# Kernel tuning notes

Measured on AMD Instinct MI355X. Metric: run time of the kernel, lower is better.

## Reference

```python
import jax, jax.numpy as jnp
import numpy as np

DIM = 2048
HQ = 32
HKV = 8
HEAD_DIM = DIM // HQ          # 64
GROUP = HQ // HKV             # 4 q-heads per kv-head
B, S = 2, 2048


def setup_inputs() -> dict:
    key = jax.random.key(0)
    ks = jax.random.split(key, 12)
    sc_in = 1.0 / np.sqrt(DIM)   # lecun_normal fan-in scaling
    inp = {
        "q": jax.random.normal(ks[0], (B, S, DIM), jnp.float32),
        "k": jax.random.normal(ks[1], (B, S, DIM), jnp.float32),
        "v": jax.random.normal(ks[2], (B, S, DIM), jnp.float32),
        # causal 0/1 mask: module computes scores -= 1/mask + 1, so 0 -> -inf (masked), 1 -> -2 (softmax-invariant shift)
        "mask": jnp.tril(jnp.ones((S, S), jnp.int32)),
        "Wq": jax.random.normal(ks[3], (DIM, HQ * HEAD_DIM), jnp.float32) * sc_in,
        "bq": jnp.zeros((HQ * HEAD_DIM,), jnp.float32),
        "Wk": jax.random.normal(ks[4], (DIM, HKV * HEAD_DIM), jnp.float32) * sc_in,
        "bk": jnp.zeros((HKV * HEAD_DIM,), jnp.float32),
        "Wv": jax.random.normal(ks[5], (DIM, HKV * HEAD_DIM), jnp.float32) * sc_in,
        "bv": jnp.zeros((HKV * HEAD_DIM,), jnp.float32),
        "Wo": jax.random.normal(ks[6], (DIM, DIM), jnp.float32) * (1.0 / np.sqrt(DIM)),
        "bo": jnp.zeros((DIM,), jnp.float32),
    }
    return inp


def reference(q, k, v, mask, Wq, bq, Wk, bk, Wv, bv, Wo, bo):
    b, s, _ = q.shape
    # projections -> per-head layout
    qx = (q @ Wq + bq).reshape(b, s, HKV, GROUP, HEAD_DIM)   # grouped q-heads
    kx = (k @ Wk + bk).reshape(b, s, HKV, HEAD_DIM)
    vx = (v @ Wv + bv).reshape(b, s, HKV, HEAD_DIM)
    # scores[b, h, g, i, j] = q_i . k_j ; same math as repeating kv heads GROUP times
    scores = jnp.einsum('bihgd,bjhd->bhgij', qx, kx) / jnp.sqrt(
        jnp.asarray(HEAD_DIM, qx.dtype))
    # module's masking: scores -= 1/mask + 1  (mask==0 -> -inf, mask==1 -> -2)
    scores = scores - (1.0 / mask.astype(scores.dtype) + 1.0)
    probs = jax.nn.softmax(scores, axis=-1)
    out = jnp.einsum('bhgij,bjhd->bihgd', probs, vx).reshape(b, s, DIM)
    out = out @ Wo + bo
    return out
```

## Files before the change

kernel.cpp:

```cpp
#include <hip/hip_runtime.h>

typedef unsigned short u16;
typedef unsigned int u32;
typedef __attribute__((ext_vector_type(8))) short short8v;
typedef __attribute__((ext_vector_type(4))) float f32x4;

#define DIM 2048
#define HQN 32
#define HKVN 8
#define HD 64
#define BB 2
#define SS 2048
#define MTOT (BB*SS)
#define NKV (HKVN*HD)
#define QSCL 0.18033688011112042f

__device__ __forceinline__ u16 f2bf(float f){
  u32 u = __float_as_uint(f);
  u += 0x7FFFu + ((u >> 16) & 1u);
  return (u16)(u >> 16);
}

__device__ __forceinline__ u32 cvtpk(float a, float b){
  u32 r; asm("v_cvt_pk_bf16_f32 %0, %1, %2" : "=v"(r) : "v"(a), "v"(b)); return r;
}

__device__ __forceinline__ void gload_lds16(const void* g, void* l){
  __builtin_amdgcn_global_load_lds((const __attribute__((address_space(1))) u32*)g,
                                   (__attribute__((address_space(3))) u32*)l, 16, 0, 0);
}

#define WAITVM_(N) asm volatile("s_waitcnt vmcnt(" #N ")" ::: "memory")
#define WAITVM(N) WAITVM_(N)
#define BARF()    do { asm volatile("" ::: "memory"); __builtin_amdgcn_s_barrier(); asm volatile("" ::: "memory"); } while(0)
#define MF(a,b,cc) __builtin_amdgcn_mfma_f32_16x16x32_bf16((a),(b),(cc),0,0,0)

__global__ __launch_bounds__(256) void cast3_kernel(const float4* __restrict__ q,
                                                    const float4* __restrict__ k,
                                                    const float4* __restrict__ v,
                                                    u16* __restrict__ qo,
                                                    u16* __restrict__ ko,
                                                    u16* __restrict__ vo, int n4){
  const int z = blockIdx.y;
  const float4* in = z==0 ? q : (z==1 ? k : v);
  u16* out = z==0 ? qo : (z==1 ? ko : vo);
  int i = blockIdx.x*256 + threadIdx.x;
  if (i < n4){
    float4 f = in[i];
    union { u16 s[4]; unsigned long long u; } r;
    r.s[0]=f2bf(f.x); r.s[1]=f2bf(f.y); r.s[2]=f2bf(f.z); r.s[3]=f2bf(f.w);
    *(unsigned long long*)(out + (size_t)i*4) = r.u;
  }
}

__global__ __launch_bounds__(256) void transpose4_kernel(const float* __restrict__ Wq,
                                                         const float* __restrict__ Wk,
                                                         const float* __restrict__ Wv,
                                                         const float* __restrict__ Wo,
                                                         u16* __restrict__ WqT,
                                                         u16* __restrict__ WkT,
                                                         u16* __restrict__ WvT,
                                                         u16* __restrict__ WoT){
  const int z = blockIdx.z;
  const float* W = z==0?Wq:(z==1?Wk:(z==2?Wv:Wo));
  u16* WT = z==0?WqT:(z==1?WkT:(z==2?WvT:WoT));
  const int N = (z==1||z==2) ? NKV : DIM;
  const int K = DIM;
  int n0 = blockIdx.x*32, k0 = blockIdx.y*32;
  if (n0 >= N) return;
  __shared__ float tile[32][33];
  int tx = threadIdx.x & 31, ty = threadIdx.x >> 5;
  #pragma unroll
  for (int i=0;i<4;i++){
    int kk = ty + i*8;
    tile[kk][tx] = W[(size_t)(k0+kk)*N + n0 + tx];
  }
  __syncthreads();
  #pragma unroll
  for (int i=0;i<4;i++){
    int n = ty + i*8;
    WT[(size_t)(n0+n)*K + k0 + tx] = f2bf(tile[tx][n]);
  }
}

__global__ __launch_bounds__(512, 1) void gemm_qkv_kernel(const u16* __restrict__ Aq,
                                                          const u16* __restrict__ Ak,
                                                          const u16* __restrict__ Av,
                                                          const u16* __restrict__ BT,
                                                          const float* __restrict__ bq,
                                                          const float* __restrict__ bk,
                                                          const float* __restrict__ bv,
                                                          u16* __restrict__ Qp,
                                                          u16* __restrict__ Kp,
                                                          u16* __restrict__ Vp){
  __shared__ __align__(16) u16 lds[65536];
  char* ldsb = (char*)lds;
  const int t = threadIdx.x, lane = t & 63, w = t >> 6;
  const int wm = w >> 2, wn = w & 3, g = lane >> 4, c = lane & 15;
  int bid = blockIdx.x;
  bid = (bid & 7)*24 + (bid >> 3);
  const int mt = bid / 12, nt = bid - mt*12;
  const int m0 = mt*256, n0 = nt*256;
  const int seg = (n0 >= 2560) ? 2 : (n0 >= 2048 ? 1 : 0);
  const u16* A = seg==0 ? Aq : (seg==1 ? Ak : Av);
  const float* bias = seg==0 ? bq : (seg==1 ? bk : bv);
  const int nbase = seg==0 ? 0 : (seg==1 ? 2048 : 2560);

  const int rA = t >> 3;
  const int kc = ((t & 7) ^ (rA & 7)) * 8;
  const u16* gA = A  + (size_t)(m0 + rA)*DIM + kc;
  const u16* gB = BT + (size_t)(n0 + ((rA>>5)<<6) + (rA & 31))*DIM + kc;

  const u32 ko0 = (u32)((g*16) ^ ((c&7)<<4));
  const u32 ko1 = (u32)((64 + g*16) ^ ((c&7)<<4));
  const u32 aoff = wm*8192 + c*128;
  const u32 boff = wn*4096 + c*128;

#define STGA_(PA, KT, ABASE) do{ \
    gload_lds16(gA + (size_t)(KT)*64 + (size_t)((PA)*64)*DIM,       ldsb + (ABASE) + (PA)*16384 + t*16); \
    gload_lds16(gA + (size_t)(KT)*64 + (size_t)((PA)*64+128)*DIM,   ldsb + (ABASE) + (PA)*16384 + 8192 + t*16); }while(0)
#define STGB_(PB, KT, BBASE) do{ \
    gload_lds16(gB + (size_t)(KT)*64 + (size_t)((PB)*32)*DIM,       ldsb + (BBASE) + (PB)*16384 + t*16); \
    gload_lds16(gB + (size_t)(KT)*64 + (size_t)((PB)*32+128)*DIM,   ldsb + (BBASE) + (PB)*16384 + 8192 + t*16); }while(0)
#define LD8(OFF) (*(const short8v*)(ldsb + (OFF)))

  const f32x4 fzero = {0.f,0.f,0.f,0.f};
  f32x4 acc[8][4];
  #pragma unroll
  for (int i=0;i<8;i++)
    #pragma unroll
    for (int j=0;j<4;j++) acc[i][j] = fzero;

#define RD_A(PABASE) do{ _Pragma("unroll") for (int q=0;q<4;q++){ \
    a_[q][0] = LD8((PABASE) + aoff + q*2048 + ko0); \
    a_[q][1] = LD8((PABASE) + aoff + q*2048 + ko1); } }while(0)
#define RD_B(DST, PBBASE) do{ _Pragma("unroll") for (int s=0;s<2;s++){ \
    DST[s][0] = LD8((PBBASE) + boff + s*2048 + ko0); \
    DST[s][1] = LD8((PBBASE) + boff + s*2048 + ko1); } }while(0)

#define MM16(BSRC, FM0, FN0) do{ __builtin_amdgcn_s_setprio(1); \
    _Pragma("unroll") for (int q=0;q<4;q++) \
      _Pragma("unroll") for (int s=0;s<2;s++){ \
        acc[(FM0)+q][(FN0)+s] = MF(a_[q][0], BSRC[s][0], acc[(FM0)+q][(FN0)+s]); \
        acc[(FM0)+q][(FN0)+s] = MF(a_[q][1], BSRC[s][1], acc[(FM0)+q][(FN0)+s]); } \
    __builtin_amdgcn_s_setprio(0); }while(0)

#define QSTEP(TT, CUR, DOSTG, TAIL) do{ \
    const u32 AC = (CUR)*32768,  BC2 = 65536 + (CUR)*32768; \
    const u32 AN = (CUR^1)*32768, BN2 = 65536 + (CUR^1)*32768; \
    short8v a_[4][2], b0_[2][2], b1_[2][2]; \
     \
    RD_A(AC); RD_B(b0_, BC2); \
    if (DOSTG) STGA_(0, (TT)+1, AN); \
    MM16(b0_, 0, 0); \
    if (TAIL) { WAITVM(2); } else { WAITVM(4); } \
    BARF(); \
     \
    RD_B(b1_, BC2 + 16384); \
    if (DOSTG) STGB_(0, (TT)+1, BN2); \
    MM16(b1_, 0, 2); \
    if (TAIL) { WAITVM(0); } else { WAITVM(4); } \
    BARF(); \
     \
    RD_A(AC + 16384); \
    if (DOSTG) STGB_(1, (TT)+1, BN2); \
    MM16(b1_, 4, 2); \
    BARF(); \
     \
    if (DOSTG) STGA_(1, (TT)+1, AN); \
    MM16(b0_, 4, 0); \
    if (!TAIL) { WAITVM(4); } \
    BARF(); \
  }while(0)

  STGA_(0, 0, 0); STGB_(0, 0, 65536); STGB_(1, 0, 65536); STGA_(1, 0, 0);
  WAITVM(4);
  BARF();

  #pragma unroll 1
  for (int tt = 0; tt < 30; tt += 2){
    QSTEP(tt,   0, 1, 0);
    QSTEP(tt+1, 1, 1, 0);
  }
  QSTEP(30, 0, 1, 0);
  QSTEP(31, 1, 0, 1);
#undef QSTEP

  WAITVM(0);
  __syncthreads();

  u16* st = lds + w*8192;
  const float osc = (seg == 0) ? QSCL : 1.0f;
  if (seg == 2){
    #pragma unroll
    for (int fm=0; fm<8; fm++){
      #pragma unroll
      for (int fn=0; fn<4; fn++){
        float bvv = bias[n0 - nbase + wn*64 + fn*16 + c];
        int vbase = (fm>>1)*2048 + fn*512 + (g*16 + c)*8 + (fm&1)*4;
        *(u32*)&st[vbase]     = cvtpk(acc[fm][fn][0]+bvv, acc[fm][fn][1]+bvv);
        *(u32*)&st[vbase + 2] = cvtpk(acc[fm][fn][2]+bvv, acc[fm][fn][3]+bvv);
      }
    }
  } else {
    #pragma unroll
    for (int fm=0; fm<8; fm++){
      #pragma unroll
      for (int fn=0; fn<4; fn++){
        float bvv = bias[n0 - nbase + wn*64 + fn*16 + c];
        int sbase = (fm>>1)*2048 + ((fm&1)*2 + (fn>>1))*512 + (c>>2)*128 + (fn&1)*4 + (c&3);
        #pragma unroll
        for (int r=0; r<4; r++)
          st[sbase + (4*g + r)*8] = f2bf((acc[fm][fn][r] + bvv)*osc);
      }
    }
  }
  __syncthreads();
  {
    const int bb = m0 >> 11;
    const int st0 = ((m0 & 2047) >> 5) + wm*4;
    u16* dst;
    if (seg == 0)      dst = Qp + (((size_t)bb*HQN  + (n0>>6)        + wn) << 17);
    else if (seg == 1) dst = Kp + (((size_t)bb*HKVN + ((n0-2048)>>6) + wn) << 17);
    else               dst = Vp + (((size_t)bb*HKVN + ((n0-2560)>>6) + wn) << 17);
    dst += (size_t)st0*2048;
    #pragma unroll
    for (int i=0;i<16;i++)
      *(short8v*)(dst + lane*8 + i*512) = *(const short8v*)(st + lane*8 + i*512);
  }
#undef STGA_
#undef STGB_
#undef RD_A
#undef RD_B
#undef MM16
}

__global__ __launch_bounds__(512, 1) void gemm_o_kernel(const u16* __restrict__ A,
                                                        const u16* __restrict__ BT,
                                                        const float* __restrict__ bias,
                                                        float* __restrict__ C){
  __shared__ __align__(16) u16 lds[49152];
  char* ldsb = (char*)lds;
  const int t = threadIdx.x, lane = t & 63, w = t >> 6;
  const int wm = w >> 2, wn = w & 3, g = lane >> 4, c = lane & 15;
  int bid = blockIdx.x;
  bid = (bid & 7)*32 + (bid >> 3);
  const int m0 = (bid >> 4)*256, n0 = (bid & 15)*128;

  const int rA = t >> 3;
  const int kc = ((t & 7) ^ (rA & 7)) * 8;
  const u16* gA = A  + (size_t)(m0 + rA)*DIM + kc;
  const u16* gB = BT + (size_t)(n0 + rA)*DIM + kc;

  const u32 ko0 = (u32)((g*16) ^ ((c&7)<<4));
  const u32 ko1 = (u32)((64 + g*16) ^ ((c&7)<<4));
  const u32 aoff = wm*8192 + c*128;
  const u32 boffo = wn*4096 + c*128;

#define STGA_(PA, KT, ABASE) do{ \
    gload_lds16(gA + (size_t)(KT)*64 + (size_t)((PA)*64)*DIM,       ldsb + (ABASE) + (PA)*16384 + t*16); \
    gload_lds16(gA + (size_t)(KT)*64 + (size_t)((PA)*64+128)*DIM,   ldsb + (ABASE) + (PA)*16384 + 8192 + t*16); }while(0)
#define STGB_O(KT, BBASE) do{ \
    gload_lds16(gB + (size_t)(KT)*64,                     ldsb + (BBASE) + t*16); \
    gload_lds16(gB + (size_t)(KT)*64 + (size_t)64*DIM,    ldsb + (BBASE) + 8192 + t*16); }while(0)
#define LD8(OFF) (*(const short8v*)(ldsb + (OFF)))

  const f32x4 fzero = {0.f,0.f,0.f,0.f};
  f32x4 acc[8][2];
  #pragma unroll
  for (int i=0;i<8;i++){ acc[i][0] = fzero; acc[i][1] = fzero; }

#define RD_A(PABASE) do{ _Pragma("unroll") for (int q=0;q<4;q++){ \
    a_[q][0] = LD8((PABASE) + aoff + q*2048 + ko0); \
    a_[q][1] = LD8((PABASE) + aoff + q*2048 + ko1); } }while(0)
#define RD_BO(BBASE) do{ _Pragma("unroll") for (int s=0;s<2;s++){ \
    b_[s][0] = LD8((BBASE) + boffo + s*2048 + ko0); \
    b_[s][1] = LD8((BBASE) + boffo + s*2048 + ko1); } }while(0)

#define MMO(FM0) do{ __builtin_amdgcn_s_setprio(1); \
    _Pragma("unroll") for (int q=0;q<4;q++) \
      _Pragma("unroll") for (int s=0;s<2;s++){ \
        acc[(FM0)+q][s] = MF(a_[q][0], b_[s][0], acc[(FM0)+q][s]); \
        acc[(FM0)+q][s] = MF(a_[q][1], b_[s][1], acc[(FM0)+q][s]); } \
    __builtin_amdgcn_s_setprio(0); }while(0)

#define OSTEP(TT, CUR, DOSTG, TAIL) do{ \
    const u32 AC = (CUR)*32768,  BC2 = 65536 + (CUR)*16384; \
    const u32 AN = (CUR^1)*32768, BN2 = 65536 + (CUR^1)*16384; \
    short8v a_[4][2], b_[2][2]; \
     \
    RD_A(AC); RD_BO(BC2); \
    if (DOSTG) { STGA_(0, (TT)+1, AN); STGB_O((TT)+1, BN2); } \
    MMO(0); \
    if (TAIL) { WAITVM(0); } else { WAITVM(4); } \
    BARF(); \
     \
    RD_A(AC + 16384); \
    if (DOSTG) STGA_(1, (TT)+1, AN); \
    MMO(4); \
    if (!TAIL) { WAITVM(2); } \
    BARF(); \
  }while(0)

  STGA_(0, 0, 0); STGB_O(0, 65536); STGA_(1, 0, 0);
  WAITVM(2);
  BARF();

  #pragma unroll 1
  for (int tt = 0; tt < 30; tt += 2){
    OSTEP(tt,   0, 1, 0);
    OSTEP(tt+1, 1, 1, 0);
  }
  OSTEP(30, 0, 1, 0);
  OSTEP(31, 1, 0, 1);
#undef OSTEP

  #pragma unroll
  for (int fm=0; fm<8; fm++){
    #pragma unroll
    for (int s=0; s<2; s++){
      int n = n0 + wn*32 + s*16 + c;
      float bvv = bias[n];
      #pragma unroll
      for (int r=0; r<4; r++){
        int m = m0 + wm*128 + fm*16 + 4*g + r;
        C[(size_t)m*DIM + n] = acc[fm][s][r] + bvv;
      }
    }
  }
#undef STGA_
#undef STGB_O
#undef RD_A
#undef RD_BO
#undef MMO
}

__global__ __launch_bounds__(256) void attn_kernel(const u16* __restrict__ Qp,
                                                   const u16* __restrict__ Kp,
                                                   const u16* __restrict__ Vp,
                                                   u16* __restrict__ Aout){
  const int bid = blockIdx.x;
  const int grp = bid & 15;
  const int T   = 63 - (bid >> 4);
  const int b   = grp >> 3;
  const int hkv = grp & 7;
  const int t = threadIdx.x;
  const int lane = t & 63, w = t >> 6;
  const int g = lane >> 4, c = lane & 15;
  const int hq = hkv*4 + w;

  __shared__ __align__(16) u16 ring[4][2][2048];

  const u16* Kb = Kp + (((size_t)b*HKVN + hkv) << 17);
  const u16* Vb = Vp + (((size_t)b*HKVN + hkv) << 17);
  const u16* Qb = Qp + (((size_t)b*HQN + hq) << 17);
  const f32x4 fzero = {0.f,0.f,0.f,0.f};

  short8v qf[2][2];
  {
    const u16* qs = Qb + (size_t)T*2048 + lane*8;
    qf[0][0] = *(const short8v*)(qs);
    qf[0][1] = *(const short8v*)(qs + 512);
    qf[1][0] = *(const short8v*)(qs + 1024);
    qf[1][1] = *(const short8v*)(qs + 1536);
  }
  float l_r[2] = {0.f, 0.f};
  f32x4 o[2][4];
  #pragma unroll
  for (int qi=0; qi<2; qi++)
    #pragma unroll
    for (int f=0; f<4; f++) o[qi][f] = fzero;

  #pragma unroll
  for (int s=0; s<3; s++){
    const int tc = s > T ? T : s;
    gload_lds16(Kb + (size_t)tc*2048 + t*8, &ring[s][0][t*8]);
    gload_lds16(Vb + (size_t)tc*2048 + t*8, &ring[s][1][t*8]);
  }

  for (int kt = 0; kt <= T; kt += 4){
    #pragma unroll
    for (int s4 = 0; s4 < 4; ++s4){
      const int kt_ = kt + s4;
      if (kt_ > T) break;
      WAITVM(4);
      BARF();
      short8v kf0 = *(const short8v*)&ring[s4][0][lane*8];
      short8v kf1 = *(const short8v*)&ring[s4][0][512 + lane*8];
      short8v kf2 = *(const short8v*)&ring[s4][0][1024 + lane*8];
      short8v kf3 = *(const short8v*)&ring[s4][0][1536 + lane*8];
      short8v vf0 = *(const short8v*)&ring[s4][1][lane*8];
      short8v vf1 = *(const short8v*)&ring[s4][1][512 + lane*8];
      short8v vf2 = *(const short8v*)&ring[s4][1][1024 + lane*8];
      short8v vf3 = *(const short8v*)&ring[s4][1][1536 + lane*8];
      {
        const int tc = (kt_+3) > T ? T : (kt_+3);
        const int sn = (s4+3) & 3;
        gload_lds16(Kb + (size_t)tc*2048 + t*8, &ring[sn][0][t*8]);
        gload_lds16(Vb + (size_t)tc*2048 + t*8, &ring[sn][1][t*8]);
      }
      const bool diag = (kt_ == T);
      #pragma unroll
      for (int qi=0; qi<2; qi++){
        f32x4 s0 = fzero, s1 = fzero;
        __builtin_amdgcn_s_setprio(1);
        s0 = MF(kf0, qf[qi][0], s0);
        s0 = MF(kf1, qf[qi][1], s0);
        s1 = MF(kf2, qf[qi][0], s1);
        s1 = MF(kf3, qf[qi][1], s1);
        __builtin_amdgcn_s_setprio(0);
        float p0[4], p1[4];
        #pragma unroll
        for (int r=0; r<4; r++){
          p0[r] = __builtin_amdgcn_exp2f(s0[r]);
          p1[r] = __builtin_amdgcn_exp2f(s1[r]);
        }
        if (diag){
          const int qloc = qi*16 + c;
          #pragma unroll
          for (int r=0; r<4; r++){
            if (4*g + r      > qloc) p0[r] = 0.f;
            if (16 + 4*g + r > qloc) p1[r] = 0.f;
          }
        }
        l_r[qi] += (p0[0]+p0[1]) + (p0[2]+p0[3]) + (p1[0]+p1[1]) + (p1[2]+p1[3]);
        union { u32 u[4]; short8v v; } pu;
        pu.u[0] = cvtpk(p0[0], p0[1]);
        pu.u[1] = cvtpk(p0[2], p0[3]);
        pu.u[2] = cvtpk(p1[0], p1[1]);
        pu.u[3] = cvtpk(p1[2], p1[3]);
        __builtin_amdgcn_s_setprio(1);
        o[qi][0] = MF(pu.v, vf0, o[qi][0]);
        o[qi][1] = MF(pu.v, vf1, o[qi][1]);
        o[qi][2] = MF(pu.v, vf2, o[qi][2]);
        o[qi][3] = MF(pu.v, vf3, o[qi][3]);
        __builtin_amdgcn_s_setprio(0);
      }
    }
  }

  #pragma unroll
  for (int qi=0; qi<2; qi++){
    float ls = l_r[qi];
    ls += __shfl_xor(ls, 16);
    ls += __shfl_xor(ls, 32);
    float li = 1.0f / ls;
    float lf[4];
    #pragma unroll
    for (int r=0; r<4; r++) lf[r] = __shfl(li, 4*g + r);
    #pragma unroll
    for (int f=0; f<4; f++){
      #pragma unroll
      for (int r=0; r<4; r++){
        int q = T*32 + qi*16 + 4*g + r;
        Aout[((size_t)b*SS + q)*DIM + hq*HD + f*16 + c] = f2bf(o[qi][f][r]*lf[r]);
      }
    }
  }
}

extern "C" void kernel_launch(void* const* d_in, const int* in_sizes, int n_in,
                              void* d_out, int out_size, void* d_ws, size_t ws_size,
                              hipStream_t stream){
  const float* q  = (const float*)d_in[0];
  const float* k  = (const float*)d_in[1];
  const float* v  = (const float*)d_in[2];
  const float* Wq = (const float*)d_in[4];
  const float* bq = (const float*)d_in[5];
  const float* Wk = (const float*)d_in[6];
  const float* bk = (const float*)d_in[7];
  const float* Wv = (const float*)d_in[8];
  const float* bv = (const float*)d_in[9];
  const float* Wo = (const float*)d_in[10];
  const float* bo = (const float*)d_in[11];
  float* out = (float*)d_out;

  char* ws = (char*)d_ws;
  u16* q_bf = (u16*)ws; ws += (size_t)MTOT*DIM*2;
  u16* k_bf = (u16*)ws; ws += (size_t)MTOT*DIM*2;
  u16* v_bf = (u16*)ws; ws += (size_t)MTOT*DIM*2;
  u16* WqT  = (u16*)ws; ws += (size_t)DIM*DIM*2;
  u16* WkT  = (u16*)ws; ws += (size_t)NKV*DIM*2;
  u16* WvT  = (u16*)ws; ws += (size_t)NKV*DIM*2;
  u16* WoT  = (u16*)ws; ws += (size_t)DIM*DIM*2;
  u16* Qp   = (u16*)ws; ws += (size_t)MTOT*DIM*2;
  u16* Kp   = (u16*)ws; ws += (size_t)MTOT*NKV*2;
  u16* Vp   = (u16*)ws; ws += (size_t)MTOT*NKV*2;
  u16* attn = (u16*)ws; ws += (size_t)MTOT*DIM*2;

  const int n4 = MTOT*DIM/4;
  cast3_kernel<<<dim3(n4/256, 3), 256, 0, stream>>>((const float4*)q, (const float4*)k,
                                                    (const float4*)v, q_bf, k_bf, v_bf, n4);
  transpose4_kernel<<<dim3(DIM/32, DIM/32, 4), 256, 0, stream>>>(Wq, Wk, Wv, Wo,
                                                                 WqT, WkT, WvT, WoT);
  gemm_qkv_kernel<<<192, 512, 0, stream>>>(q_bf, k_bf, v_bf, WqT,
                                           bq, bk, bv, Qp, Kp, Vp);
  attn_kernel<<<1024, 256, 0, stream>>>(Qp, Kp, Vp, attn);
  gemm_o_kernel<<<256, 512, 0, stream>>>(attn, WoT, bo, out);
}
```

Baseline: 187.3 us.

## Shrink QKV and O GEMM tiles to 128x128 with two blocks per CU

```diff
diff --git a/kernel.cpp b/kernel.cpp
--- a/kernel.cpp
+++ b/kernel.cpp
@@ -83,7 +83,7 @@
   }
 }
 
-__global__ __launch_bounds__(512, 1) void gemm_qkv_kernel(const u16* __restrict__ Aq,
+__global__ __launch_bounds__(256, 2) void gemm_qkv_kernel(const u16* __restrict__ Aq,
                                                           const u16* __restrict__ Ak,
                                                           const u16* __restrict__ Av,
                                                           const u16* __restrict__ BT,
@@ -93,107 +93,103 @@
                                                           u16* __restrict__ Qp,
                                                           u16* __restrict__ Kp,
                                                           u16* __restrict__ Vp){
-  __shared__ __align__(16) u16 lds[65536];
+  __shared__ __align__(16) u16 lds[32768];
   char* ldsb = (char*)lds;
   const int t = threadIdx.x, lane = t & 63, w = t >> 6;
-  const int wm = w >> 2, wn = w & 3, g = lane >> 4, c = lane & 15;
+  const int wm = w >> 1, wn = w & 1, g = lane >> 4, c = lane & 15;
   int bid = blockIdx.x;
-  bid = (bid & 7)*24 + (bid >> 3);
-  const int mt = bid / 12, nt = bid - mt*12;
-  const int m0 = mt*256, n0 = nt*256;
-  const int seg = (n0 >= 2560) ? 2 : (n0 >= 2048 ? 1 : 0);
+  bid = (bid & 7)*96 + (bid >> 3);
+  const int mI = bid/24, nidx = bid - mI*24;
+  const int m0 = mI*128;
+  int seg, n0;
+  if (nidx < 16){ seg = 0; n0 = nidx*128; }
+  else if (nidx < 20){ seg = 1; n0 = 2048 + (nidx-16)*128; }
+  else { seg = 2; n0 = 2560 + (nidx-20)*128; }
   const u16* A = seg==0 ? Aq : (seg==1 ? Ak : Av);
   const float* bias = seg==0 ? bq : (seg==1 ? bk : bv);
   const int nbase = seg==0 ? 0 : (seg==1 ? 2048 : 2560);
 
-  const int rA = t >> 3;
-  const int kc = ((t & 7) ^ (rA & 7)) * 8;
-  const u16* gA = A  + (size_t)(m0 + rA)*DIM + kc;
-  const u16* gB = BT + (size_t)(n0 + ((rA>>5)<<6) + (rA & 31))*DIM + kc;
+  const int rS = t >> 3;
+  const int kc = ((t & 7) ^ (rS & 7)) * 8;
+  const u16* gA = A  + (size_t)(m0 + rS)*DIM + kc;
+  const u16* gB = BT + (size_t)(n0 + rS)*DIM + kc;
 
   const u32 ko0 = (u32)((g*16) ^ ((c&7)<<4));
   const u32 ko1 = (u32)((64 + g*16) ^ ((c&7)<<4));
   const u32 aoff = wm*8192 + c*128;
-  const u32 boff = wn*4096 + c*128;
-
-#define STGA_(PA, KT, ABASE) do{ \
-    gload_lds16(gA + (size_t)(KT)*64 + (size_t)((PA)*64)*DIM,       ldsb + (ABASE) + (PA)*16384 + t*16); \
-    gload_lds16(gA + (size_t)(KT)*64 + (size_t)((PA)*64+128)*DIM,   ldsb + (ABASE) + (PA)*16384 + 8192 + t*16); }while(0)
-#define STGB_(PB, KT, BBASE) do{ \
-    gload_lds16(gB + (size_t)(KT)*64 + (size_t)((PB)*32)*DIM,       ldsb + (BBASE) + (PB)*16384 + t*16); \
-    gload_lds16(gB + (size_t)(KT)*64 + (size_t)((PB)*32+128)*DIM,   ldsb + (BBASE) + (PB)*16384 + 8192 + t*16); }while(0)
+  const u32 boff = wn*8192 + c*128;
+
+#define STG_A(KT, AB) do{ size_t ko_=(size_t)(KT)*64; \
+    gload_lds16(gA + ko_,                ldsb + (AB) +         t*16); \
+    gload_lds16(gA + ko_ + (size_t)32*DIM, ldsb + (AB) + 4096  + t*16); \
+    gload_lds16(gA + ko_ + (size_t)64*DIM, ldsb + (AB) + 8192  + t*16); \
+    gload_lds16(gA + ko_ + (size_t)96*DIM, ldsb + (AB) + 12288 + t*16); }while(0)
+#define STG_B(KT, BB) do{ size_t ko_=(size_t)(KT)*64; \
+    gload_lds16(gB + ko_,                ldsb + (BB) +         t*16); \
+    gload_lds16(gB + ko_ + (size_t)64*DIM, ldsb + (BB) + 8192  + t*16); \
+    gload_lds16(gB + ko_ + (size_t)32*DIM, ldsb + (BB) + 4096  + t*16); \
+    gload_lds16(gB + ko_ + (size_t)96*DIM, ldsb + (BB) + 12288 + t*16); }while(0)
 #define LD8(OFF) (*(const short8v*)(ldsb + (OFF)))
 
   const f32x4 fzero = {0.f,0.f,0.f,0.f};
-  f32x4 acc[8][4];
-  #pragma unroll
-  for (int i=0;i<8;i++)
+  f32x4 acc[4][4];
+  #pragma unroll
+  for (int i=0;i<4;i++)
     #pragma unroll
     for (int j=0;j<4;j++) acc[i][j] = fzero;
 
-#define RD_A(PABASE) do{ _Pragma("unroll") for (int q=0;q<4;q++){ \
-    a_[q][0] = LD8((PABASE) + aoff + q*2048 + ko0); \
-    a_[q][1] = LD8((PABASE) + aoff + q*2048 + ko1); } }while(0)
-#define RD_B(DST, PBBASE) do{ _Pragma("unroll") for (int s=0;s<2;s++){ \
-    DST[s][0] = LD8((PBBASE) + boff + s*2048 + ko0); \
-    DST[s][1] = LD8((PBBASE) + boff + s*2048 + ko1); } }while(0)
-
-#define MM16(BSRC, FM0, FN0) do{ __builtin_amdgcn_s_setprio(1); \
+#define TILE(TT, CUR, DOSTG, TAIL) do{ \
+    const u32 AC = (CUR)*16384, BC = 32768 + (CUR)*16384; \
+    const u32 AN = (CUR^1)*16384, BN = 32768 + (CUR^1)*16384; \
+    short8v a_[4][2], b_[4][2]; \
+    WAITVM(2); \
+    BARF(); \
+    _Pragma("unroll") for (int q=0;q<4;q++){ \
+      a_[q][0] = LD8(AC + aoff + q*2048 + ko0); \
+      a_[q][1] = LD8(AC + aoff + q*2048 + ko1); } \
+    b_[0][0] = LD8(BC + boff + ko0);        b_[0][1] = LD8(BC + boff + ko1); \
+    b_[1][0] = LD8(BC + boff + 2048 + ko0); b_[1][1] = LD8(BC + boff + 2048 + ko1); \
+    if (DOSTG) STG_A((TT)+1, AN); \
+    __builtin_amdgcn_s_setprio(1); \
     _Pragma("unroll") for (int q=0;q<4;q++) \
       _Pragma("unroll") for (int s=0;s<2;s++){ \
-        acc[(FM0)+q][(FN0)+s] = MF(a_[q][0], BSRC[s][0], acc[(FM0)+q][(FN0)+s]); \
-        acc[(FM0)+q][(FN0)+s] = MF(a_[q][1], BSRC[s][1], acc[(FM0)+q][(FN0)+s]); } \
-    __builtin_amdgcn_s_setprio(0); }while(0)
-
-#define QSTEP(TT, CUR, DOSTG, TAIL) do{ \
-    const u32 AC = (CUR)*32768,  BC2 = 65536 + (CUR)*32768; \
-    const u32 AN = (CUR^1)*32768, BN2 = 65536 + (CUR^1)*32768; \
-    short8v a_[4][2], b0_[2][2], b1_[2][2]; \
-     \
-    RD_A(AC); RD_B(b0_, BC2); \
-    if (DOSTG) STGA_(0, (TT)+1, AN); \
-    MM16(b0_, 0, 0); \
-    if (TAIL) { WAITVM(2); } else { WAITVM(4); } \
-    BARF(); \
-     \
-    RD_B(b1_, BC2 + 16384); \
-    if (DOSTG) STGB_(0, (TT)+1, BN2); \
-    MM16(b1_, 0, 2); \
+        acc[q][s] = MF(a_[q][0], b_[s][0], acc[q][s]); \
+        acc[q][s] = MF(a_[q][1], b_[s][1], acc[q][s]); } \
+    __builtin_amdgcn_s_setprio(0); \
     if (TAIL) { WAITVM(0); } else { WAITVM(4); } \
     BARF(); \
-     \
-    RD_A(AC + 16384); \
-    if (DOSTG) STGB_(1, (TT)+1, BN2); \
-    MM16(b1_, 4, 2); \
-    BARF(); \
-     \
-    if (DOSTG) STGA_(1, (TT)+1, AN); \
-    MM16(b0_, 4, 0); \
-    if (!TAIL) { WAITVM(4); } \
-    BARF(); \
+    b_[2][0] = LD8(BC + boff + 4096 + ko0); b_[2][1] = LD8(BC + boff + 4096 + ko1); \
+    b_[3][0] = LD8(BC + boff + 6144 + ko0); b_[3][1] = LD8(BC + boff + 6144 + ko1); \
+    if (DOSTG) STG_B((TT)+1, BN); \
+    __builtin_amdgcn_s_setprio(1); \
+    _Pragma("unroll") for (int q=0;q<4;q++) \
+      _Pragma("unroll") for (int s=2;s<4;s++){ \
+        acc[q][s] = MF(a_[q][0], b_[s][0], acc[q][s]); \
+        acc[q][s] = MF(a_[q][1], b_[s][1], acc[q][s]); } \
+    __builtin_amdgcn_s_setprio(0); \
   }while(0)
 
-  STGA_(0, 0, 0); STGB_(0, 0, 65536); STGB_(1, 0, 65536); STGA_(1, 0, 0);
-  WAITVM(4);
-  BARF();
+  STG_A(0, 0); STG_B(0, 32768);
 
   #pragma unroll 1
   for (int tt = 0; tt < 30; tt += 2){
-    QSTEP(tt,   0, 1, 0);
-    QSTEP(tt+1, 1, 1, 0);
-  }
-  QSTEP(30, 0, 1, 0);
-  QSTEP(31, 1, 0, 1);
-#undef QSTEP
+    TILE(tt,   0, 1, 0);
+    TILE(tt+1, 1, 1, 0);
+  }
+  TILE(30, 0, 1, 0);
+  TILE(31, 1, 0, 1);
+#undef TILE
+#undef STG_A
+#undef STG_B
 
   WAITVM(0);
   __syncthreads();
 
-  u16* st = lds + w*8192;
+  u16* st = lds + w*4096;
   const float osc = (seg == 0) ? QSCL : 1.0f;
   if (seg == 2){
     #pragma unroll
-    for (int fm=0; fm<8; fm++){
+    for (int fm=0; fm<4; fm++){
       #pragma unroll
       for (int fn=0; fn<4; fn++){
         float bvv = bias[n0 - nbase + wn*64 + fn*16 + c];
@@ -204,7 +200,7 @@
     }
   } else {
     #pragma unroll
-    for (int fm=0; fm<8; fm++){
+    for (int fm=0; fm<4; fm++){
       #pragma unroll
       for (int fn=0; fn<4; fn++){
         float bvv = bias[n0 - nbase + wn*64 + fn*16 + c];
@@ -218,121 +214,118 @@
   __syncthreads();
   {
     const int bb = m0 >> 11;
-    const int st0 = ((m0 & 2047) >> 5) + wm*4;
+    const int st0 = ((m0 & 2047) >> 5) + wm*2;
     u16* dst;
     if (seg == 0)      dst = Qp + (((size_t)bb*HQN  + (n0>>6)        + wn) << 17);
     else if (seg == 1) dst = Kp + (((size_t)bb*HKVN + ((n0-2048)>>6) + wn) << 17);
     else               dst = Vp + (((size_t)bb*HKVN + ((n0-2560)>>6) + wn) << 17);
     dst += (size_t)st0*2048;
     #pragma unroll
-    for (int i=0;i<16;i++)
+    for (int i=0;i<8;i++)
       *(short8v*)(dst + lane*8 + i*512) = *(const short8v*)(st + lane*8 + i*512);
   }
-#undef STGA_
-#undef STGB_
-#undef RD_A
-#undef RD_B
-#undef MM16
-}
-
-__global__ __launch_bounds__(512, 1) void gemm_o_kernel(const u16* __restrict__ A,
+#undef LD8
+}
+
+__global__ __launch_bounds__(256, 2) void gemm_o_kernel(const u16* __restrict__ A,
                                                         const u16* __restrict__ BT,
                                                         const float* __restrict__ bias,
                                                         float* __restrict__ C){
-  __shared__ __align__(16) u16 lds[49152];
+  __shared__ __align__(16) u16 lds[32768];
   char* ldsb = (char*)lds;
   const int t = threadIdx.x, lane = t & 63, w = t >> 6;
-  const int wm = w >> 2, wn = w & 3, g = lane >> 4, c = lane & 15;
+  const int wm = w >> 1, wn = w & 1, g = lane >> 4, c = lane & 15;
   int bid = blockIdx.x;
-  bid = (bid & 7)*32 + (bid >> 3);
-  const int m0 = (bid >> 4)*256, n0 = (bid & 15)*128;
-
-  const int rA = t >> 3;
-  const int kc = ((t & 7) ^ (rA & 7)) * 8;
-  const u16* gA = A  + (size_t)(m0 + rA)*DIM + kc;
-  const u16* gB = BT + (size_t)(n0 + rA)*DIM + kc;
+  bid = (bid & 7)*64 + (bid >> 3);
+  const int m0 = (bid >> 4)*128, n0 = (bid & 15)*128;
+
+  const int rS = t >> 3;
+  const int kc = ((t & 7) ^ (rS & 7)) * 8;
+  const u16* gA = A  + (size_t)(m0 + rS)*DIM + kc;
+  const u16* gB = BT + (size_t)(n0 + rS)*DIM + kc;
 
   const u32 ko0 = (u32)((g*16) ^ ((c&7)<<4));
   const u32 ko1 = (u32)((64 + g*16) ^ ((c&7)<<4));
   const u32 aoff = wm*8192 + c*128;
-  const u32 boffo = wn*4096 + c*128;
-
-#define STGA_(PA, KT, ABASE) do{ \
-    gload_lds16(gA + (size_t)(KT)*64 + (size_t)((PA)*64)*DIM,       ldsb + (ABASE) + (PA)*16384 + t*16); \
-    gload_lds16(gA + (size_t)(KT)*64 + (size_t)((PA)*64+128)*DIM,   ldsb + (ABASE) + (PA)*16384 + 8192 + t*16); }while(0)
-#define STGB_O(KT, BBASE) do{ \
-    gload_lds16(gB + (size_t)(KT)*64,                     ldsb + (BBASE) + t*16); \
-    gload_lds16(gB + (size_t)(KT)*64 + (size_t)64*DIM,    ldsb + (BBASE) + 8192 + t*16); }while(0)
+  const u32 boff = wn*8192 + c*128;
+
+#define STG_A(KT, AB) do{ size_t ko_=(size_t)(KT)*64; \
+    gload_lds16(gA + ko_,                ldsb + (AB) +         t*16); \
+    gload_lds16(gA + ko_ + (size_t)32*DIM, ldsb + (AB) + 4096  + t*16); \
+    gload_lds16(gA + ko_ + (size_t)64*DIM, ldsb + (AB) + 8192  + t*16); \
+    gload_lds16(gA + ko_ + (size_t)96*DIM, ldsb + (AB) + 12288 + t*16); }while(0)
+#define STG_B(KT, BB) do{ size_t ko_=(size_t)(KT)*64; \
+    gload_lds16(gB + ko_,                ldsb + (BB) +         t*16); \
+    gload_lds16(gB + ko_ + (size_t)64*DIM, ldsb + (BB) + 8192  + t*16); \
+    gload_lds16(gB + ko_ + (size_t)32*DIM, ldsb + (BB) + 4096  + t*16); \
+    gload_lds16(gB + ko_ + (size_t)96*DIM, ldsb + (BB) + 12288 + t*16); }while(0)
 #define LD8(OFF) (*(const short8v*)(ldsb + (OFF)))
 
   const f32x4 fzero = {0.f,0.f,0.f,0.f};
-  f32x4 acc[8][2];
-  #pragma unroll
-  for (int i=0;i<8;i++){ acc[i][0] = fzero; acc[i][1] = fzero; }
-
-#define RD_A(PABASE) do{ _Pragma("unroll") for (int q=0;q<4;q++){ \
-    a_[q][0] = LD8((PABASE) + aoff + q*2048 + ko0); \
-    a_[q][1] = LD8((PABASE) + aoff + q*2048 + ko1); } }while(0)
-#define RD_BO(BBASE) do{ _Pragma("unroll") for (int s=0;s<2;s++){ \
-    b_[s][0] = LD8((BBASE) + boffo + s*2048 + ko0); \
-    b_[s][1] = LD8((BBASE) + boffo + s*2048 + ko1); } }while(0)
-
-#define MMO(FM0) do{ __builtin_amdgcn_s_setprio(1); \
+  f32x4 acc[4][4];
+  #pragma unroll
+  for (int i=0;i<4;i++)
+    #pragma unroll
+    for (int j=0;j<4;j++) acc[i][j] = fzero;
+
+#define TILE(TT, CUR, DOSTG, TAIL) do{ \
+    const u32 AC = (CUR)*16384, BC = 32768 + (CUR)*16384; \
+    const u32 AN = (CUR^1)*16384, BN = 32768 + (CUR^1)*16384; \
+    short8v a_[4][2], b_[4][2]; \
+    WAITVM(2); \
+    BARF(); \
+    _Pragma("unroll") for (int q=0;q<4;q++){ \
+      a_[q][0] = LD8(AC + aoff + q*2048 + ko0); \
+      a_[q][1] = LD8(AC + aoff + q*2048 + ko1); } \
+    b_[0][0] = LD8(BC + boff + ko0);        b_[0][1] = LD8(BC + boff + ko1); \
+    b_[1][0] = LD8(BC + boff + 2048 + ko0); b_[1][1] = LD8(BC + boff + 2048 + ko1); \
+    if (DOSTG) STG_A((TT)+1, AN); \
+    __builtin_amdgcn_s_setprio(1); \
     _Pragma("unroll") for (int q=0;q<4;q++) \
       _Pragma("unroll") for (int s=0;s<2;s++){ \
-        acc[(FM0)+q][s] = MF(a_[q][0], b_[s][0], acc[(FM0)+q][s]); \
-        acc[(FM0)+q][s] = MF(a_[q][1], b_[s][1], acc[(FM0)+q][s]); } \
-    __builtin_amdgcn_s_setprio(0); }while(0)
-
-#define OSTEP(TT, CUR, DOSTG, TAIL) do{ \
-    const u32 AC = (CUR)*32768,  BC2 = 65536 + (CUR)*16384; \
-    const u32 AN = (CUR^1)*32768, BN2 = 65536 + (CUR^1)*16384; \
-    short8v a_[4][2], b_[2][2]; \
-     \
-    RD_A(AC); RD_BO(BC2); \
-    if (DOSTG) { STGA_(0, (TT)+1, AN); STGB_O((TT)+1, BN2); } \
-    MMO(0); \
+        acc[q][s] = MF(a_[q][0], b_[s][0], acc[q][s]); \
+        acc[q][s] = MF(a_[q][1], b_[s][1], acc[q][s]); } \
+    __builtin_amdgcn_s_setprio(0); \
     if (TAIL) { WAITVM(0); } else { WAITVM(4); } \
     BARF(); \
-     \
-    RD_A(AC + 16384); \
-    if (DOSTG) STGA_(1, (TT)+1, AN); \
-    MMO(4); \
-    if (!TAIL) { WAITVM(2); } \
-    BARF(); \
+    b_[2][0] = LD8(BC + boff + 4096 + ko0); b_[2][1] = LD8(BC + boff + 4096 + ko1); \
+    b_[3][0] = LD8(BC + boff + 6144 + ko0); b_[3][1] = LD8(BC + boff + 6144 + ko1); \
+    if (DOSTG) STG_B((TT)+1, BN); \
+    __builtin_amdgcn_s_setprio(1); \
+    _Pragma("unroll") for (int q=0;q<4;q++) \
+      _Pragma("unroll") for (int s=2;s<4;s++){ \
+        acc[q][s] = MF(a_[q][0], b_[s][0], acc[q][s]); \
+        acc[q][s] = MF(a_[q][1], b_[s][1], acc[q][s]); } \
+    __builtin_amdgcn_s_setprio(0); \
   }while(0)
 
-  STGA_(0, 0, 0); STGB_O(0, 65536); STGA_(1, 0, 0);
-  WAITVM(2);
-  BARF();
+  STG_A(0, 0); STG_B(0, 32768);
 
   #pragma unroll 1
   for (int tt = 0; tt < 30; tt += 2){
-    OSTEP(tt,   0, 1, 0);
-    OSTEP(tt+1, 1, 1, 0);
-  }
-  OSTEP(30, 0, 1, 0);
-  OSTEP(31, 1, 0, 1);
-#undef OSTEP
-
-  #pragma unroll
-  for (int fm=0; fm<8; fm++){
-    #pragma unroll
-    for (int s=0; s<2; s++){
-      int n = n0 + wn*32 + s*16 + c;
+    TILE(tt,   0, 1, 0);
+    TILE(tt+1, 1, 1, 0);
+  }
+  TILE(30, 0, 1, 0);
+  TILE(31, 1, 0, 1);
+#undef TILE
+#undef STG_A
+#undef STG_B
+#undef LD8
+
+  #pragma unroll
+  for (int fm=0; fm<4; fm++){
+    #pragma unroll
+    for (int fn=0; fn<4; fn++){
+      int n = n0 + wn*64 + fn*16 + c;
       float bvv = bias[n];
       #pragma unroll
       for (int r=0; r<4; r++){
-        int m = m0 + wm*128 + fm*16 + 4*g + r;
-        C[(size_t)m*DIM + n] = acc[fm][s][r] + bvv;
+        int m = m0 + wm*64 + fm*16 + 4*g + r;
+        C[(size_t)m*DIM + n] = acc[fm][fn][r] + bvv;
       }
     }
   }
-#undef STGA_
-#undef STGB_O
-#undef RD_A
-#undef RD_BO
-#undef MMO
 }
 
 __global__ __launch_bounds__(256) void attn_kernel(const u16* __restrict__ Qp,
@@ -493,8 +486,8 @@
                                                     (const float4*)v, q_bf, k_bf, v_bf, n4);
   transpose4_kernel<<<dim3(DIM/32, DIM/32, 4), 256, 0, stream>>>(Wq, Wk, Wv, Wo,
                                                                  WqT, WkT, WvT, WoT);
-  gemm_qkv_kernel<<<192, 512, 0, stream>>>(q_bf, k_bf, v_bf, WqT,
+  gemm_qkv_kernel<<<768, 256, 0, stream>>>(q_bf, k_bf, v_bf, WqT,
                                            bq, bk, bv, Qp, Kp, Vp);
   attn_kernel<<<1024, 256, 0, stream>>>(Qp, Kp, Vp, attn);
-  gemm_o_kernel<<<256, 512, 0, stream>>>(attn, WoT, bo, out);
-}
+  gemm_o_kernel<<<512, 256, 0, stream>>>(attn, WoT, bo, out);
+}
```

New measurement: 195.1 us. 4.2% more time.
